# Kernel optimization log

Measured on AMD Instinct MI355X. Metric: run time of the kernel, lower is better.

Reference implementation:

```python
import jax, jax.numpy as jnp
import numpy as np


def _grid_sample_3d(x, grid):
    """Trilinear 3D grid_sample, align_corners=False, zero padding.
    x: [B,C,D,H,W]; grid: [B,D,H,W,3] with (gx,gy,gz) in [-1,1] indexing (W,H,D).
    """
    B, C, D, H, W = x.shape
    gx, gy, gz = grid[..., 0], grid[..., 1], grid[..., 2]
    # unnormalize (align_corners=False)
    ix = ((gx + 1.0) * W - 1.0) * 0.5
    iy = ((gy + 1.0) * H - 1.0) * 0.5
    iz = ((gz + 1.0) * D - 1.0) * 0.5
    ix0f = jnp.floor(ix); iy0f = jnp.floor(iy); iz0f = jnp.floor(iz)
    fx = ix - ix0f; fy = iy - iy0f; fz = iz - iz0f
    ix0 = ix0f.astype(jnp.int32); iy0 = iy0f.astype(jnp.int32); iz0 = iz0f.astype(jnp.int32)
    N = D * H * W
    x_flat = x.reshape(B, C, N)
    out = jnp.zeros_like(x)
    for dz in (0, 1):
        for dy in (0, 1):
            for dx in (0, 1):
                xi = ix0 + dx; yi = iy0 + dy; zi = iz0 + dz
                w = ((fx if dx else 1.0 - fx)
                     * (fy if dy else 1.0 - fy)
                     * (fz if dz else 1.0 - fz))
                valid = ((xi >= 0) & (xi < W) & (yi >= 0) & (yi < H)
                         & (zi >= 0) & (zi < D))
                xc = jnp.clip(xi, 0, W - 1)
                yc = jnp.clip(yi, 0, H - 1)
                zc = jnp.clip(zi, 0, D - 1)
                idx = (zc * H + yc) * W + xc  # [B,D,H,W]
                g = jnp.take_along_axis(x_flat, idx.reshape(B, 1, N), axis=2)
                g = g.reshape(B, C, D, H, W)
                out = out + g * (w * valid)[:, None]
    return out


def setup_inputs() -> dict:
    key = jax.random.key(0)
    k1, k2, k3, k4 = jax.random.split(key, 4)
    B, C, D, H, W = 8, 4, 128, 128, 128
    F_DIM = 512
    x = jax.random.normal(k1, (B, C, D, H, W), dtype=jnp.float32)
    im_feat = jax.random.normal(k2, (B, F_DIM), dtype=jnp.float32)
    pos_w = jax.random.normal(k3, (2, F_DIM), dtype=jnp.float32) * 0.02
    pos_b = jax.random.normal(k4, (2,), dtype=jnp.float32) * 0.02
    return {"x": x, "im_feat": im_feat, "pos_w": pos_w, "pos_b": pos_b}


def reference(x, im_feat, pos_w, pos_b):
    B, C, D, H, W = x.shape
    mu_rho = im_feat @ pos_w.T + pos_b  # [B,2]
    mu, rho = mu_rho[:, 0], mu_rho[:, 1]
    cm, sm = jnp.cos(mu), jnp.sin(mu)
    cr, sr = jnp.cos(rho), jnp.sin(rho)
    zero = jnp.zeros_like(mu); one = jnp.ones_like(mu)
    # rotation about x-axis by rho, about y-axis by mu: [B,3,3]
    rot_x = jnp.stack([
        jnp.stack([one, zero, zero], -1),
        jnp.stack([zero, cr, sr], -1),
        jnp.stack([zero, -sr, cr], -1)], -2)
    rot_y = jnp.stack([
        jnp.stack([cm, zero, -sm], -1),
        jnp.stack([zero, one, zero], -1),
        jnp.stack([sm, zero, cm], -1)], -2)
    R = jnp.einsum('bij,bjk->bik', rot_y, rot_x)
    X = jnp.linspace(-1.0, 1.0, W, dtype=x.dtype)
    Y = jnp.linspace(-1.0, 1.0, H, dtype=x.dtype)
    Z = jnp.linspace(-1.0, 1.0, D, dtype=x.dtype)
    zz, yy, xx = jnp.meshgrid(Z, Y, X, indexing='ij')  # [D,H,W]
    coords = jnp.stack([xx, yy, zz], -1)               # [D,H,W,3]
    grid = jnp.einsum('bij,dhwj->bdhwi', R, coords)    # [B,D,H,W,3]
    return _grid_sample_3d(x, grid)
```

## Files before the change

### kernel.cpp

```cpp
#include <hip/hip_runtime.h>

#define DHW (128*128*128)

__global__ void compute_R_kernel(const float* __restrict__ im_feat,
                                 const float* __restrict__ pos_w,
                                 const float* __restrict__ pos_b,
                                 float* __restrict__ Rout) {
    int b = blockIdx.x;
    int t = threadIdx.x;
    const float* f = im_feat + b * 512;
    float s0 = 0.f, s1 = 0.f;
    for (int i = t; i < 512; i += 64) {
        float v = f[i];
        s0 = fmaf(v, pos_w[i], s0);
        s1 = fmaf(v, pos_w[512 + i], s1);
    }
    for (int off = 32; off > 0; off >>= 1) {
        s0 += __shfl_down(s0, off, 64);
        s1 += __shfl_down(s1, off, 64);
    }
    if (t == 0) {
        float mu  = s0 + pos_b[0];
        float rho = s1 + pos_b[1];
        float cm = cosf(mu),  sm = sinf(mu);
        float cr = cosf(rho), sr = sinf(rho);
        float* R = Rout + b * 16;
        R[0] = cm;   R[1] = sm * sr;  R[2] = -sm * cr;
        R[3] = 0.f;  R[4] = cr;       R[5] = sr;
        R[6] = sm;   R[7] = -cm * sr; R[8] = cm * cr;
    }
}

__global__ __launch_bounds__(256) void transpose_kernel(const float* __restrict__ x,
                                                        float4* __restrict__ xt) {
    unsigned tid = blockIdx.x * 256u + threadIdx.x;
    unsigned spatial = tid & (DHW - 1u);
    unsigned b = tid >> 21;
    const float* xb = x + (size_t)(b << 2) * DHW;
    float a0 = xb[spatial];
    float a1 = xb[spatial + DHW];
    float a2 = xb[spatial + 2u * DHW];
    float a3 = xb[spatial + 3u * DHW];
    xt[(size_t)tid] = make_float4(a0, a1, a2, a3);
}

__global__ __launch_bounds__(256) void sample_kernel_t(const float4* __restrict__ xt,
                                                       const float* __restrict__ Rin,
                                                       float* __restrict__ out) {
    unsigned bid = blockIdx.x;
    int b = (int)(bid >> 13);
    unsigned spatial = ((bid & 8191u) << 8) | threadIdx.x;

    int w = spatial & 127;
    int h = (spatial >> 7) & 127;
    int d = spatial >> 14;

    const float* R = Rin + b * 16;
    const float step = 2.0f / 127.0f;
    float X = fmaf((float)w, step, -1.0f);
    float Y = fmaf((float)h, step, -1.0f);
    float Z = fmaf((float)d, step, -1.0f);

    float gx = fmaf(R[0], X, fmaf(R[1], Y, R[2] * Z));
    float gy = fmaf(R[4], Y, R[5] * Z);
    float gz = fmaf(R[6], X, fmaf(R[7], Y, R[8] * Z));

    float ix = fmaf(gx, 64.0f, 63.5f);
    float iy = fmaf(gy, 64.0f, 63.5f);
    float iz = fmaf(gz, 64.0f, 63.5f);

    float fx0 = floorf(ix), fy0 = floorf(iy), fz0 = floorf(iz);
    float fx = ix - fx0, fy = iy - fy0, fz = iz - fz0;
    int ix0 = (int)fx0, iy0 = (int)fy0, iz0 = (int)fz0;
    int ix1 = ix0 + 1, iy1 = iy0 + 1, iz1 = iz0 + 1;

    float wx0 = ((unsigned)ix0 < 128u) ? (1.f - fx) : 0.f;
    float wx1 = ((unsigned)ix1 < 128u) ? fx : 0.f;
    float wy0 = ((unsigned)iy0 < 128u) ? (1.f - fy) : 0.f;
    float wy1 = ((unsigned)iy1 < 128u) ? fy : 0.f;
    float wz0 = ((unsigned)iz0 < 128u) ? (1.f - fz) : 0.f;
    float wz1 = ((unsigned)iz1 < 128u) ? fz : 0.f;

    float* ob = out + (size_t)(b << 2) * DHW + spatial;

    if ((wx0 + wx1) * (wy0 + wy1) * (wz0 + wz1) == 0.f) {
        __builtin_nontemporal_store(0.f, ob);
        __builtin_nontemporal_store(0.f, ob + DHW);
        __builtin_nontemporal_store(0.f, ob + 2 * DHW);
        __builtin_nontemporal_store(0.f, ob + 3 * DHW);
        return;
    }

    int xc0 = min(max(ix0, 0), 127), xc1 = min(max(ix1, 0), 127);
    int yc0 = min(max(iy0, 0), 127), yc1 = min(max(iy1, 0), 127);
    int zc0 = min(max(iz0, 0), 127), zc1 = min(max(iz1, 0), 127);

    int r00 = (zc0 * 128 + yc0) * 128;
    int r01 = (zc0 * 128 + yc1) * 128;
    int r10 = (zc1 * 128 + yc0) * 128;
    int r11 = (zc1 * 128 + yc1) * 128;

    const float4* xb = xt + (size_t)b * DHW;

    float4 q0 = xb[r00 + xc0], q1 = xb[r00 + xc1];
    float4 q2 = xb[r01 + xc0], q3 = xb[r01 + xc1];
    float4 q4 = xb[r10 + xc0], q5 = xb[r10 + xc1];
    float4 q6 = xb[r11 + xc0], q7 = xb[r11 + xc1];

    float w00 = wz0 * wy0, w01 = wz0 * wy1, w10 = wz1 * wy0, w11 = wz1 * wy1;

    float a0, a1, a2, a3;
    a0 = (q0.x * wx0 + q1.x * wx1) * w00;
    a1 = (q0.y * wx0 + q1.y * wx1) * w00;
    a2 = (q0.z * wx0 + q1.z * wx1) * w00;
    a3 = (q0.w * wx0 + q1.w * wx1) * w00;

    a0 = fmaf(q2.x * wx0 + q3.x * wx1, w01, a0);
    a1 = fmaf(q2.y * wx0 + q3.y * wx1, w01, a1);
    a2 = fmaf(q2.z * wx0 + q3.z * wx1, w01, a2);
    a3 = fmaf(q2.w * wx0 + q3.w * wx1, w01, a3);

    a0 = fmaf(q4.x * wx0 + q5.x * wx1, w10, a0);
    a1 = fmaf(q4.y * wx0 + q5.y * wx1, w10, a1);
    a2 = fmaf(q4.z * wx0 + q5.z * wx1, w10, a2);
    a3 = fmaf(q4.w * wx0 + q5.w * wx1, w10, a3);

    a0 = fmaf(q6.x * wx0 + q7.x * wx1, w11, a0);
    a1 = fmaf(q6.y * wx0 + q7.y * wx1, w11, a1);
    a2 = fmaf(q6.z * wx0 + q7.z * wx1, w11, a2);
    a3 = fmaf(q6.w * wx0 + q7.w * wx1, w11, a3);

    __builtin_nontemporal_store(a0, ob);
    __builtin_nontemporal_store(a1, ob + DHW);
    __builtin_nontemporal_store(a2, ob + 2 * DHW);
    __builtin_nontemporal_store(a3, ob + 3 * DHW);
}

__global__ __launch_bounds__(256) void sample_kernel(const float* __restrict__ x,
                                                     const float* __restrict__ Rin,
                                                     float* __restrict__ out) {
    unsigned bid = blockIdx.x;
    int b = (int)(bid >> 13);
    unsigned spatial = ((bid & 8191u) << 8) | threadIdx.x;

    int w = spatial & 127;
    int h = (spatial >> 7) & 127;
    int d = spatial >> 14;

    const float* R = Rin + b * 16;
    const float step = 2.0f / 127.0f;
    float X = fmaf((float)w, step, -1.0f);
    float Y = fmaf((float)h, step, -1.0f);
    float Z = fmaf((float)d, step, -1.0f);

    float gx = fmaf(R[0], X, fmaf(R[1], Y, R[2] * Z));
    float gy = fmaf(R[4], Y, R[5] * Z);
    float gz = fmaf(R[6], X, fmaf(R[7], Y, R[8] * Z));

    float ix = fmaf(gx, 64.0f, 63.5f);
    float iy = fmaf(gy, 64.0f, 63.5f);
    float iz = fmaf(gz, 64.0f, 63.5f);

    float fx0 = floorf(ix), fy0 = floorf(iy), fz0 = floorf(iz);
    float fx = ix - fx0, fy = iy - fy0, fz = iz - fz0;
    int ix0 = (int)fx0, iy0 = (int)fy0, iz0 = (int)fz0;
    int ix1 = ix0 + 1, iy1 = iy0 + 1, iz1 = iz0 + 1;

    float wx0 = ((unsigned)ix0 < 128u) ? (1.f - fx) : 0.f;
    float wx1 = ((unsigned)ix1 < 128u) ? fx : 0.f;
    float wy0 = ((unsigned)iy0 < 128u) ? (1.f - fy) : 0.f;
    float wy1 = ((unsigned)iy1 < 128u) ? fy : 0.f;
    float wz0 = ((unsigned)iz0 < 128u) ? (1.f - fz) : 0.f;
    float wz1 = ((unsigned)iz1 < 128u) ? fz : 0.f;

    float* ob = out + (size_t)(b << 2) * DHW + spatial;

    if ((wx0 + wx1) * (wy0 + wy1) * (wz0 + wz1) == 0.f) {
        __builtin_nontemporal_store(0.f, ob);
        __builtin_nontemporal_store(0.f, ob + DHW);
        __builtin_nontemporal_store(0.f, ob + 2 * DHW);
        __builtin_nontemporal_store(0.f, ob + 3 * DHW);
        return;
    }

    int xc0 = min(max(ix0, 0), 127), xc1 = min(max(ix1, 0), 127);
    int yc0 = min(max(iy0, 0), 127), yc1 = min(max(iy1, 0), 127);
    int zc0 = min(max(iz0, 0), 127), zc1 = min(max(iz1, 0), 127);

    int r00 = (zc0 * 128 + yc0) * 128;
    int r01 = (zc0 * 128 + yc1) * 128;
    int r10 = (zc1 * 128 + yc0) * 128;
    int r11 = (zc1 * 128 + yc1) * 128;

    int o0 = r00 + xc0, o1 = r00 + xc1;
    int o2 = r01 + xc0, o3 = r01 + xc1;
    int o4 = r10 + xc0, o5 = r10 + xc1;
    int o6 = r11 + xc0, o7 = r11 + xc1;

    const float* xb = x + (size_t)(b << 2) * DHW;

    float v[4][8];
#pragma unroll
    for (int c = 0; c < 4; ++c) {
        const float* xc = xb + (size_t)c * DHW;
        v[c][0] = xc[o0]; v[c][1] = xc[o1];
        v[c][2] = xc[o2]; v[c][3] = xc[o3];
        v[c][4] = xc[o4]; v[c][5] = xc[o5];
        v[c][6] = xc[o6]; v[c][7] = xc[o7];
    }

    float w00 = wz0 * wy0, w01 = wz0 * wy1, w10 = wz1 * wy0, w11 = wz1 * wy1;

#pragma unroll
    for (int c = 0; c < 4; ++c) {
        float acc;
        acc  = (v[c][0] * wx0 + v[c][1] * wx1) * w00;
        acc += (v[c][2] * wx0 + v[c][3] * wx1) * w01;
        acc += (v[c][4] * wx0 + v[c][5] * wx1) * w10;
        acc += (v[c][6] * wx0 + v[c][7] * wx1) * w11;
        __builtin_nontemporal_store(acc, ob + (size_t)c * DHW);
    }
}

extern "C" void kernel_launch(void* const* d_in, const int* in_sizes, int n_in,
                              void* d_out, int out_size, void* d_ws, size_t ws_size,
                              hipStream_t stream) {
    const float* x       = (const float*)d_in[0];
    const float* im_feat = (const float*)d_in[1];
    const float* pos_w   = (const float*)d_in[2];
    const float* pos_b   = (const float*)d_in[3];
    float* out = (float*)d_out;

    float* Rws = (float*)d_ws;
    const size_t XT_OFF = 1024;
    size_t need = XT_OFF + (size_t)8 * 4 * DHW * sizeof(float);

    compute_R_kernel<<<8, 64, 0, stream>>>(im_feat, pos_w, pos_b, Rws);

    int total = 8 * DHW;
    if (ws_size >= need) {
        float4* xt = (float4*)((char*)d_ws + XT_OFF);
        transpose_kernel<<<total / 256, 256, 0, stream>>>(x, xt);
        sample_kernel_t<<<total / 256, 256, 0, stream>>>(xt, Rws, out);
    } else {
        sample_kernel<<<total / 256, 256, 0, stream>>>(x, Rws, out);
    }
}
```

Measured before the change: 639.8 us.

## Pack transposed input as fp16 and fetch x-neighbour pairs with single 16-byte loads

The channel-interleaved copy of x is now stored as fp16 (8 bytes per voxel instead of 16), which halves the size of the intermediate buffer and the bytes read per gather. Both x-neighbours are fetched with one dwordx4 load starting at a clamped base column, so each sample issues 4 loads instead of 8, with weights remapped for the clamped edge. h and d are marked wave-uniform with readfirstlane. The trade-off is fp16 rounding of the inputs, which may break tolerance, plus inline asm with a forced waitcnt that limits how the compiler can schedule the loads.

```diff
diff --git a/kernel.cpp b/kernel.cpp
--- a/kernel.cpp
+++ b/kernel.cpp
@@ -1,6 +1,9 @@
 #include <hip/hip_runtime.h>
+#include <hip/hip_fp16.h>
 
 #define DHW (128*128*128)
+
+typedef unsigned int u32x4 __attribute__((ext_vector_type(4)));
 
 __global__ void compute_R_kernel(const float* __restrict__ im_feat,
                                  const float* __restrict__ pos_w,
@@ -31,20 +34,29 @@
     }
 }
 
-__global__ __launch_bounds__(256) void transpose_kernel(const float* __restrict__ x,
-                                                        float4* __restrict__ xt) {
+__global__ __launch_bounds__(256) void transpose_pack_kernel(const float* __restrict__ x,
+                                                             uint2* __restrict__ xt) {
     unsigned tid = blockIdx.x * 256u + threadIdx.x;
     unsigned spatial = tid & (DHW - 1u);
     unsigned b = tid >> 21;
-    const float* xb = x + (size_t)(b << 2) * DHW;
-    float a0 = xb[spatial];
-    float a1 = xb[spatial + DHW];
-    float a2 = xb[spatial + 2u * DHW];
-    float a3 = xb[spatial + 3u * DHW];
-    xt[(size_t)tid] = make_float4(a0, a1, a2, a3);
-}
-
-__global__ __launch_bounds__(256) void sample_kernel_t(const float4* __restrict__ xt,
+    const float* xb = x + (size_t)(b << 2) * DHW + spatial;
+    float a0 = xb[0];
+    float a1 = xb[DHW];
+    float a2 = xb[2u * DHW];
+    float a3 = xb[3u * DHW];
+    unsigned lo = (unsigned)__half_as_ushort(__float2half_rn(a0)) |
+                  ((unsigned)__half_as_ushort(__float2half_rn(a1)) << 16);
+    unsigned hi = (unsigned)__half_as_ushort(__float2half_rn(a2)) |
+                  ((unsigned)__half_as_ushort(__float2half_rn(a3)) << 16);
+    xt[(size_t)tid] = make_uint2(lo, hi);
+}
+
+__device__ inline float2 up2(unsigned u) {
+    __half2 h = reinterpret_cast<const __half2&>(u);
+    return __half22float2(h);
+}
+
+__global__ __launch_bounds__(256) void sample_kernel_h(const char* __restrict__ xt,
                                                        const float* __restrict__ Rin,
                                                        float* __restrict__ out) {
     unsigned bid = blockIdx.x;
@@ -54,6 +66,8 @@
     int w = spatial & 127;
     int h = (spatial >> 7) & 127;
     int d = spatial >> 14;
+    h = __builtin_amdgcn_readfirstlane(h);
+    d = __builtin_amdgcn_readfirstlane(d);
 
     const float* R = Rin + b * 16;
     const float step = 2.0f / 127.0f;
@@ -91,44 +105,62 @@
         return;
     }
 
-    int xc0 = min(max(ix0, 0), 127), xc1 = min(max(ix1, 0), 127);
     int yc0 = min(max(iy0, 0), 127), yc1 = min(max(iy1, 0), 127);
     int zc0 = min(max(iz0, 0), 127), zc1 = min(max(iz1, 0), 127);
 
-    int r00 = (zc0 * 128 + yc0) * 128;
-    int r01 = (zc0 * 128 + yc1) * 128;
-    int r10 = (zc1 * 128 + yc0) * 128;
-    int r11 = (zc1 * 128 + yc1) * 128;
-
-    const float4* xb = xt + (size_t)b * DHW;
-
-    float4 q0 = xb[r00 + xc0], q1 = xb[r00 + xc1];
-    float4 q2 = xb[r01 + xc0], q3 = xb[r01 + xc1];
-    float4 q4 = xb[r10 + xc0], q5 = xb[r10 + xc1];
-    float4 q6 = xb[r11 + xc0], q7 = xb[r11 + xc1];
+    int base = min(max(ix0, 0), 126);
+    float sw0 = (base == ix0 ? wx0 : 0.f) + (base == ix1 ? wx1 : 0.f);
+    float sw1 = (base + 1 == ix0 ? wx0 : 0.f) + (base + 1 == ix1 ? wx1 : 0.f);
+
+    const char* xb = xt + (size_t)b * (DHW * 8);
+    unsigned o00 = (((unsigned)(zc0 * 128 + yc0) << 7) + (unsigned)base) << 3;
+    unsigned o01 = (((unsigned)(zc0 * 128 + yc1) << 7) + (unsigned)base) << 3;
+    unsigned o10 = (((unsigned)(zc1 * 128 + yc0) << 7) + (unsigned)base) << 3;
+    unsigned o11 = (((unsigned)(zc1 * 128 + yc1) << 7) + (unsigned)base) << 3;
+
+    u32x4 q0, q1, q2, q3;
+    asm volatile("global_load_dwordx4 %0, %1, off" : "=v"(q0) : "v"(xb + o00));
+    asm volatile("global_load_dwordx4 %0, %1, off" : "=v"(q1) : "v"(xb + o01));
+    asm volatile("global_load_dwordx4 %0, %1, off" : "=v"(q2) : "v"(xb + o10));
+    asm volatile("global_load_dwordx4 %0, %1, off" : "=v"(q3) : "v"(xb + o11));
+    asm volatile("s_waitcnt vmcnt(0)" ::: "memory");
+    __builtin_amdgcn_sched_barrier(0);
 
     float w00 = wz0 * wy0, w01 = wz0 * wy1, w10 = wz1 * wy0, w11 = wz1 * wy1;
 
-    float a0, a1, a2, a3;
-    a0 = (q0.x * wx0 + q1.x * wx1) * w00;
-    a1 = (q0.y * wx0 + q1.y * wx1) * w00;
-    a2 = (q0.z * wx0 + q1.z * wx1) * w00;
-    a3 = (q0.w * wx0 + q1.w * wx1) * w00;
-
-    a0 = fmaf(q2.x * wx0 + q3.x * wx1, w01, a0);
-    a1 = fmaf(q2.y * wx0 + q3.y * wx1, w01, a1);
-    a2 = fmaf(q2.z * wx0 + q3.z * wx1, w01, a2);
-    a3 = fmaf(q2.w * wx0 + q3.w * wx1, w01, a3);
-
-    a0 = fmaf(q4.x * wx0 + q5.x * wx1, w10, a0);
-    a1 = fmaf(q4.y * wx0 + q5.y * wx1, w10, a1);
-    a2 = fmaf(q4.z * wx0 + q5.z * wx1, w10, a2);
-    a3 = fmaf(q4.w * wx0 + q5.w * wx1, w10, a3);
-
-    a0 = fmaf(q6.x * wx0 + q7.x * wx1, w11, a0);
-    a1 = fmaf(q6.y * wx0 + q7.y * wx1, w11, a1);
-    a2 = fmaf(q6.z * wx0 + q7.z * wx1, w11, a2);
-    a3 = fmaf(q6.w * wx0 + q7.w * wx1, w11, a3);
+    float a0 = 0.f, a1 = 0.f, a2 = 0.f, a3 = 0.f;
+    {
+        float ws0 = sw0 * w00, ws1 = sw1 * w00;
+        float2 p0 = up2(q0.x), p1 = up2(q0.y), p2 = up2(q0.z), p3 = up2(q0.w);
+        a0 = fmaf(p0.x, ws0, fmaf(p2.x, ws1, a0));
+        a1 = fmaf(p0.y, ws0, fmaf(p2.y, ws1, a1));
+        a2 = fmaf(p1.x, ws0, fmaf(p3.x, ws1, a2));
+        a3 = fmaf(p1.y, ws0, fmaf(p3.y, ws1, a3));
+    }
+    {
+        float ws0 = sw0 * w01, ws1 = sw1 * w01;
+        float2 p0 = up2(q1.x), p1 = up2(q1.y), p2 = up2(q1.z), p3 = up2(q1.w);
+        a0 = fmaf(p0.x, ws0, fmaf(p2.x, ws1, a0));
+        a1 = fmaf(p0.y, ws0, fmaf(p2.y, ws1, a1));
+        a2 = fmaf(p1.x, ws0, fmaf(p3.x, ws1, a2));
+        a3 = fmaf(p1.y, ws0, fmaf(p3.y, ws1, a3));
+    }
+    {
+        float ws0 = sw0 * w10, ws1 = sw1 * w10;
+        float2 p0 = up2(q2.x), p1 = up2(q2.y), p2 = up2(q2.z), p3 = up2(q2.w);
+        a0 = fmaf(p0.x, ws0, fmaf(p2.x, ws1, a0));
+        a1 = fmaf(p0.y, ws0, fmaf(p2.y, ws1, a1));
+        a2 = fmaf(p1.x, ws0, fmaf(p3.x, ws1, a2));
+        a3 = fmaf(p1.y, ws0, fmaf(p3.y, ws1, a3));
+    }
+    {
+        float ws0 = sw0 * w11, ws1 = sw1 * w11;
+        float2 p0 = up2(q3.x), p1 = up2(q3.y), p2 = up2(q3.z), p3 = up2(q3.w);
+        a0 = fmaf(p0.x, ws0, fmaf(p2.x, ws1, a0));
+        a1 = fmaf(p0.y, ws0, fmaf(p2.y, ws1, a1));
+        a2 = fmaf(p1.x, ws0, fmaf(p3.x, ws1, a2));
+        a3 = fmaf(p1.y, ws0, fmaf(p3.y, ws1, a3));
+    }
 
     __builtin_nontemporal_store(a0, ob);
     __builtin_nontemporal_store(a1, ob + DHW);
@@ -233,15 +265,15 @@
 
     float* Rws = (float*)d_ws;
     const size_t XT_OFF = 1024;
-    size_t need = XT_OFF + (size_t)8 * 4 * DHW * sizeof(float);
+    size_t need = XT_OFF + (size_t)8 * DHW * 8 + 64;
 
     compute_R_kernel<<<8, 64, 0, stream>>>(im_feat, pos_w, pos_b, Rws);
 
     int total = 8 * DHW;
     if (ws_size >= need) {
-        float4* xt = (float4*)((char*)d_ws + XT_OFF);
-        transpose_kernel<<<total / 256, 256, 0, stream>>>(x, xt);
-        sample_kernel_t<<<total / 256, 256, 0, stream>>>(xt, Rws, out);
+        uint2* xt = (uint2*)((char*)d_ws + XT_OFF);
+        transpose_pack_kernel<<<total / 256, 256, 0, stream>>>(x, xt);
+        sample_kernel_h<<<total / 256, 256, 0, stream>>>((const char*)xt, Rws, out);
     } else {
         sample_kernel<<<total / 256, 256, 0, stream>>>(x, Rws, out);
     }
```

New measurement: 536.6 us. -16.1%, faster.
